# Kernel tuning notes

Measured on AMD Instinct MI355X. Metric: run time of the kernel, lower is better.

The kernel has to match this reference:

```python
import jax, jax.numpy as jnp
import numpy as np

N_NODES = 100000
FEAT_DIM = 256
EMBED_DIM = 256
BATCH = 50000
NUM_SAMPLE = 10


def setup_inputs() -> dict:
    key = jax.random.key(0)
    k1, k2, k3, k4 = jax.random.split(key, 4)
    features = jax.random.normal(k1, (N_NODES, FEAT_DIM), dtype=jnp.float32)
    # weight: [embed_dim, 2*feat_dim] (gcn=False path), xavier-like scale
    weight = jax.random.normal(k2, (EMBED_DIM, 2 * FEAT_DIM), dtype=jnp.float32)
    weight = weight * jnp.sqrt(2.0 / (EMBED_DIM + 2 * FEAT_DIM))
    nodes = jax.random.randint(k3, (BATCH,), 0, N_NODES, dtype=jnp.int64)
    neigh_idx = jax.random.randint(k4, (BATCH, NUM_SAMPLE), 0, N_NODES, dtype=jnp.int64)
    return {"features": features, "weight": weight, "nodes": nodes, "neigh_idx": neigh_idx}


def reference(features, weight, nodes, neigh_idx):
    # MeanAggregator: gather sampled neighbor feats and average over samples
    neigh_feats = features[neigh_idx].mean(axis=1)          # [B, F]
    self_feats = features[nodes]                             # [B, F]
    combined = jnp.concatenate([self_feats, neigh_feats], axis=1)  # [B, 2F]
    # weight.mm(combined.t()) -> [embed_dim, B], then relu
    out = jax.nn.relu(weight @ combined.T)
    return out
```

## Files before the change

### kernel.cpp

```cpp
#include <hip/hip_runtime.h>

#define FEAT   256
#define K2     512
#define NNODES 100000
#define BATCH  50000
#define NS     10
#define EMBED  256
#define BN     32
#define NBLK   ((BATCH + BN - 1) / BN)

typedef __attribute__((ext_vector_type(8))) __bf16         bf16x8;
typedef __attribute__((ext_vector_type(8))) unsigned short ushort8;
typedef __attribute__((ext_vector_type(4))) float          f32x4;
typedef __attribute__((ext_vector_type(2))) float          f32x2;
typedef __attribute__((ext_vector_type(2))) int            i32x2;
typedef __attribute__((ext_vector_type(4))) int            i32x4;

static __device__ __forceinline__ unsigned short f2bf(float x) {
    unsigned int u = __builtin_bit_cast(unsigned int, x);
    u += 0x7FFFu + ((u >> 16) & 1u);
    return (unsigned short)(u >> 16);
}

__global__ void fconv_kernel(const float* __restrict__ f,
                             unsigned char* __restrict__ f8) {
    int i = blockIdx.x * blockDim.x + threadIdx.x;
    const f32x4* src = (const f32x4*)(f + (size_t)i * 8);
    f32x4 a = src[0], b = src[1];
    int u0 = 0, u1 = 0;
    u0 = __builtin_amdgcn_cvt_pk_fp8_f32(a[0], a[1], u0, false);
    u0 = __builtin_amdgcn_cvt_pk_fp8_f32(a[2], a[3], u0, true);
    u1 = __builtin_amdgcn_cvt_pk_fp8_f32(b[0], b[1], u1, false);
    u1 = __builtin_amdgcn_cvt_pk_fp8_f32(b[2], b[3], u1, true);
    i32x2 p; p[0] = u0; p[1] = u1;
    ((i32x2*)f8)[i] = p;
}

__global__ void wpack_kernel(const float* __restrict__ w,
                             unsigned short* __restrict__ wp) {
    int c    = blockIdx.x * blockDim.x + threadIdx.x;
    int lane = c & 63;
    int ks   = (c >> 6) & 1;
    int mblk = (c >> 7) & 15;
    int kt   = c >> 11;
    int row  = mblk * 16 + (lane & 15);
    int col  = kt * 64 + ks * 32 + (lane >> 4) * 8;
    const f32x4* src = (const f32x4*)(w + row * K2 + col);
    f32x4 a = src[0], b = src[1];
    ushort8 h;
    h[0]=f2bf(a[0]); h[1]=f2bf(a[1]); h[2]=f2bf(a[2]); h[3]=f2bf(a[3]);
    h[4]=f2bf(b[0]); h[5]=f2bf(b[1]); h[6]=f2bf(b[2]); h[7]=f2bf(b[3]);
    ((ushort8*)wp)[c] = h;
}

__global__ __launch_bounds__(512, 4) void gemm_hyb(
    const float* __restrict__ features,
    const unsigned char* __restrict__ f8,
    const unsigned short* __restrict__ wp,
    const int* __restrict__ nodes,
    const int* __restrict__ neigh,
    float* __restrict__ out) {

    __shared__ __align__(16) unsigned short lB[BN * K2];

    const int tid = threadIdx.x;
    const int nb0 = blockIdx.x * BN;
    const int r   = tid >> 4;
    const int p   = tid & 15;
    const int rx  = r & 7;
    const int n   = min(nb0 + r, BATCH - 1);

    {
        const int node0 = nodes[n];
        const f32x4* s0 = (const f32x4*)(features + (size_t)node0 * FEAT + p * 16);
        f32x4 x0 = s0[0], x1 = s0[1], x2 = s0[2], x3 = s0[3];
        ushort8 a, b;
        a[0]=f2bf(x0[0]); a[1]=f2bf(x0[1]); a[2]=f2bf(x0[2]); a[3]=f2bf(x0[3]);
        a[4]=f2bf(x1[0]); a[5]=f2bf(x1[1]); a[6]=f2bf(x1[2]); a[7]=f2bf(x1[3]);
        b[0]=f2bf(x2[0]); b[1]=f2bf(x2[1]); b[2]=f2bf(x2[2]); b[3]=f2bf(x2[3]);
        b[4]=f2bf(x3[0]); b[5]=f2bf(x3[1]); b[6]=f2bf(x3[2]); b[7]=f2bf(x3[3]);
        const int g = p >> 2, i0 = (p & 3) * 2;
        unsigned short* dst = lB + r * K2 + g * 64;
        *(ushort8*)&dst[((i0    ) ^ rx) * 8] = a;
        *(ushort8*)&dst[((i0 + 1) ^ rx) * 8] = b;
    }

    {
        int idx[NS];
        #pragma unroll
        for (int s = 0; s < NS; ++s) idx[s] = neigh[n * NS + s];

        float acc[16];
        #pragma unroll
        for (int e = 0; e < 16; ++e) acc[e] = 0.f;

        #pragma unroll
        for (int s = 0; s < NS; ++s) {
            i32x4 v = *(const i32x4*)(f8 + (size_t)idx[s] * FEAT + p * 16);
            #pragma unroll
            for (int q = 0; q < 4; ++q) {
                f32x2 lo = __builtin_amdgcn_cvt_pk_f32_fp8(v[q], false);
                f32x2 hi = __builtin_amdgcn_cvt_pk_f32_fp8(v[q], true);
                acc[q * 4 + 0] += lo[0];
                acc[q * 4 + 1] += lo[1];
                acc[q * 4 + 2] += hi[0];
                acc[q * 4 + 3] += hi[1];
            }
        }
        ushort8 a, b;
        #pragma unroll
        for (int e = 0; e < 8; ++e) {
            a[e] = f2bf(acc[e]     * 0.1f);
            b[e] = f2bf(acc[8 + e] * 0.1f);
        }
        const int g = 4 + (p >> 2), i0 = (p & 3) * 2;
        unsigned short* dst = lB + r * K2 + g * 64;
        *(ushort8*)&dst[((i0    ) ^ rx) * 8] = a;
        *(ushort8*)&dst[((i0 + 1) ^ rx) * 8] = b;
    }
    __syncthreads();

    const int w    = tid >> 6;
    const int lane = tid & 63;
    const int lr   = lane & 15;
    const int lg   = lane >> 4;

    f32x4 facc[2][2] = {};

    #pragma unroll
    for (int kt = 0; kt < 8; ++kt) {
        bf16x8 af[2][2], bfr[2][2];
        #pragma unroll
        for (int i = 0; i < 2; ++i)
            #pragma unroll
            for (int ks = 0; ks < 2; ++ks)
                af[i][ks] = *(const bf16x8*)(wp +
                    ((((kt * 16 + w * 2 + i) * 2 + ks) * 64 + lane) << 3));
        #pragma unroll
        for (int j = 0; j < 2; ++j) {
            const int rb = j * 16 + lr;
            #pragma unroll
            for (int ks = 0; ks < 2; ++ks) {
                int cc = kt * 8 + ((ks * 4 + lg) ^ (rb & 7));
                bfr[j][ks] = *(const bf16x8*)&lB[rb * K2 + cc * 8];
            }
        }
        #pragma unroll
        for (int ks = 0; ks < 2; ++ks)
            #pragma unroll
            for (int i = 0; i < 2; ++i)
                #pragma unroll
                for (int j = 0; j < 2; ++j)
                    facc[i][j] = __builtin_amdgcn_mfma_f32_16x16x32_bf16(
                        af[i][ks], bfr[j][ks], facc[i][j], 0, 0, 0);
    }

    #pragma unroll
    for (int j = 0; j < 2; ++j) {
        const int n2 = nb0 + j * 16 + lr;
        if (n2 < BATCH) {
            #pragma unroll
            for (int i = 0; i < 2; ++i) {
                int m0 = w * 32 + i * 16 + lg * 4;
                #pragma unroll
                for (int rg = 0; rg < 4; ++rg) {
                    float v = facc[i][j][rg];
                    v = v > 0.f ? v : 0.f;
                    __builtin_nontemporal_store(v, &out[(size_t)(m0 + rg) * BATCH + n2]);
                }
            }
        }
    }
}

__global__ __launch_bounds__(512, 4) void gemm_f32(
    const float* __restrict__ features,
    const unsigned short* __restrict__ wp,
    const int* __restrict__ nodes,
    const int* __restrict__ neigh,
    float* __restrict__ out) {

    __shared__ __align__(16) unsigned short lB[BN * K2];

    const int tid = threadIdx.x;
    const int nb0 = blockIdx.x * BN;
    const int r  = tid >> 4;
    const int h  = tid & 15;
    const int rx = r & 7;
    const int n  = min(nb0 + r, BATCH - 1);

    int node0 = nodes[n];
    int nidx[NS];
    #pragma unroll
    for (int s = 0; s < NS; ++s) nidx[s] = neigh[n * NS + s];

    {
        const f32x4* s0 = (const f32x4*)(features + (size_t)node0 * FEAT + h * 16);
        f32x4 x0 = s0[0], x1 = s0[1], x2 = s0[2], x3 = s0[3];
        ushort8 a, b;
        a[0]=f2bf(x0[0]); a[1]=f2bf(x0[1]); a[2]=f2bf(x0[2]); a[3]=f2bf(x0[3]);
        a[4]=f2bf(x1[0]); a[5]=f2bf(x1[1]); a[6]=f2bf(x1[2]); a[7]=f2bf(x1[3]);
        b[0]=f2bf(x2[0]); b[1]=f2bf(x2[1]); b[2]=f2bf(x2[2]); b[3]=f2bf(x2[3]);
        b[4]=f2bf(x3[0]); b[5]=f2bf(x3[1]); b[6]=f2bf(x3[2]); b[7]=f2bf(x3[3]);
        const int g = h >> 2, i0 = (h & 3) * 2;
        unsigned short* dst = lB + r * K2 + g * 64;
        *(ushort8*)&dst[((i0    ) ^ rx) * 8] = a;
        *(ushort8*)&dst[((i0 + 1) ^ rx) * 8] = b;
    }
    {
        float acc[16];
        #pragma unroll
        for (int e = 0; e < 16; ++e) acc[e] = 0.f;
        #pragma unroll
        for (int s = 0; s < NS; ++s) {
            const f32x4* pp = (const f32x4*)(features + (size_t)nidx[s] * FEAT + h * 16);
            f32x4 x0 = pp[0], x1 = pp[1], x2 = pp[2], x3 = pp[3];
            #pragma unroll
            for (int e = 0; e < 4; ++e) {
                acc[e]      += x0[e];
                acc[4 + e]  += x1[e];
                acc[8 + e]  += x2[e];
                acc[12 + e] += x3[e];
            }
        }
        ushort8 aa, bb;
        #pragma unroll
        for (int e = 0; e < 8; ++e) {
            aa[e] = f2bf(acc[e]     * 0.1f);
            bb[e] = f2bf(acc[8 + e] * 0.1f);
        }
        const int g = 4 + (h >> 2), i0 = (h & 3) * 2;
        unsigned short* dst = lB + r * K2 + g * 64;
        *(ushort8*)&dst[((i0    ) ^ rx) * 8] = aa;
        *(ushort8*)&dst[((i0 + 1) ^ rx) * 8] = bb;
    }
    __syncthreads();

    const int w    = tid >> 6;
    const int lane = tid & 63;
    const int lr   = lane & 15;
    const int lg   = lane >> 4;

    f32x4 facc[2][2] = {};
    #pragma unroll
    for (int kt = 0; kt < 8; ++kt) {
        bf16x8 af[2][2], bfr[2][2];
        #pragma unroll
        for (int i = 0; i < 2; ++i)
            #pragma unroll
            for (int ks = 0; ks < 2; ++ks)
                af[i][ks] = *(const bf16x8*)(wp +
                    ((((kt * 16 + w * 2 + i) * 2 + ks) * 64 + lane) << 3));
        #pragma unroll
        for (int j = 0; j < 2; ++j) {
            const int rb = j * 16 + lr;
            #pragma unroll
            for (int ks = 0; ks < 2; ++ks) {
                int cc = kt * 8 + ((ks * 4 + lg) ^ (rb & 7));
                bfr[j][ks] = *(const bf16x8*)&lB[rb * K2 + cc * 8];
            }
        }
        #pragma unroll
        for (int ks = 0; ks < 2; ++ks)
            #pragma unroll
            for (int i = 0; i < 2; ++i)
                #pragma unroll
                for (int j = 0; j < 2; ++j)
                    facc[i][j] = __builtin_amdgcn_mfma_f32_16x16x32_bf16(
                        af[i][ks], bfr[j][ks], facc[i][j], 0, 0, 0);
    }
    #pragma unroll
    for (int j = 0; j < 2; ++j) {
        const int n2 = nb0 + j * 16 + lr;
        if (n2 < BATCH) {
            #pragma unroll
            for (int i = 0; i < 2; ++i) {
                int m0 = w * 32 + i * 16 + lg * 4;
                #pragma unroll
                for (int rg = 0; rg < 4; ++rg) {
                    float v = facc[i][j][rg];
                    v = v > 0.f ? v : 0.f;
                    __builtin_nontemporal_store(v, &out[(size_t)(m0 + rg) * BATCH + n2]);
                }
            }
        }
    }
}

extern "C" void kernel_launch(void* const* d_in, const int* in_sizes, int n_in,
                              void* d_out, int out_size, void* d_ws, size_t ws_size,
                              hipStream_t stream) {
    const float* features = (const float*)d_in[0];
    const float* weight   = (const float*)d_in[1];
    const int*   nodes    = (const int*)d_in[2];
    const int*   neigh    = (const int*)d_in[3];
    float* out = (float*)d_out;

    unsigned short* wp = (unsigned short*)d_ws;
    unsigned char*  f8 = (unsigned char*)(wp + (size_t)EMBED * K2);

    const size_t need = (size_t)EMBED * K2 * 2 + (size_t)NNODES * FEAT;

    wpack_kernel<<<(EMBED * K2 / 8) / 256, 256, 0, stream>>>(weight, wp);

    if (ws_size >= need) {
        fconv_kernel<<<(NNODES * FEAT / 8) / 256, 256, 0, stream>>>(features, f8);
        gemm_hyb<<<NBLK, 512, 0, stream>>>(features, f8, wp, nodes, neigh, out);
    } else {
        gemm_f32<<<NBLK, 512, 0, stream>>>(features, wp, nodes, neigh, out);
    }
}
```

Before: 74.20 us.

## Double batch tile to 64 columns with 1024-thread blocks in hybrid GEMM

The hybrid gather+GEMM kernel now handles 64 batch columns per block with 1024 threads (16 waves). Each wave owns one 16-row slice of the output embedding and all four 16-column batch tiles, rather than a 32x32 tile. This halves the number of blocks and the total number of times the packed weight is reloaded, and each wave's weight fragment is reused across four batch tiles. The costs are 64 KB of LDS per block and fewer, larger blocks, which reduces occupancy and makes the tail coarser. The fallback f32 kernel keeps its 32-column tiling.

```diff
diff --git a/kernel.cpp b/kernel.cpp
--- a/kernel.cpp
+++ b/kernel.cpp
@@ -6,7 +6,7 @@
 #define BATCH  50000
 #define NS     10
 #define EMBED  256
-#define BN     32
+#define BN     64
 #define NBLK   ((BATCH + BN - 1) / BN)
 
 typedef __attribute__((ext_vector_type(8))) __bf16         bf16x8;
@@ -53,7 +53,7 @@
     ((ushort8*)wp)[c] = h;
 }
 
-__global__ __launch_bounds__(512, 4) void gemm_hyb(
+__global__ __launch_bounds__(1024, 4) void gemm_hyb(
     const float* __restrict__ features,
     const unsigned char* __restrict__ f8,
     const unsigned short* __restrict__ wp,
@@ -125,49 +125,38 @@
     const int lr   = lane & 15;
     const int lg   = lane >> 4;
 
-    f32x4 facc[2][2] = {};
+    f32x4 facc[4] = {};
 
     #pragma unroll
     for (int kt = 0; kt < 8; ++kt) {
-        bf16x8 af[2][2], bfr[2][2];
-        #pragma unroll
-        for (int i = 0; i < 2; ++i)
-            #pragma unroll
-            for (int ks = 0; ks < 2; ++ks)
-                af[i][ks] = *(const bf16x8*)(wp +
-                    ((((kt * 16 + w * 2 + i) * 2 + ks) * 64 + lane) << 3));
-        #pragma unroll
-        for (int j = 0; j < 2; ++j) {
+        bf16x8 af[2];
+        #pragma unroll
+        for (int ks = 0; ks < 2; ++ks)
+            af[ks] = *(const bf16x8*)(wp +
+                ((((kt * 16 + w) * 2 + ks) * 64 + lane) << 3));
+        #pragma unroll
+        for (int j = 0; j < 4; ++j) {
             const int rb = j * 16 + lr;
             #pragma unroll
             for (int ks = 0; ks < 2; ++ks) {
                 int cc = kt * 8 + ((ks * 4 + lg) ^ (rb & 7));
-                bfr[j][ks] = *(const bf16x8*)&lB[rb * K2 + cc * 8];
-            }
-        }
-        #pragma unroll
-        for (int ks = 0; ks < 2; ++ks)
-            #pragma unroll
-            for (int i = 0; i < 2; ++i)
-                #pragma unroll
-                for (int j = 0; j < 2; ++j)
-                    facc[i][j] = __builtin_amdgcn_mfma_f32_16x16x32_bf16(
-                        af[i][ks], bfr[j][ks], facc[i][j], 0, 0, 0);
-    }
-
-    #pragma unroll
-    for (int j = 0; j < 2; ++j) {
+                bf16x8 bfr = *(const bf16x8*)&lB[rb * K2 + cc * 8];
+                facc[j] = __builtin_amdgcn_mfma_f32_16x16x32_bf16(
+                    af[ks], bfr, facc[j], 0, 0, 0);
+            }
+        }
+    }
+
+    const int m0 = w * 16 + lg * 4;
+    #pragma unroll
+    for (int j = 0; j < 4; ++j) {
         const int n2 = nb0 + j * 16 + lr;
         if (n2 < BATCH) {
             #pragma unroll
-            for (int i = 0; i < 2; ++i) {
-                int m0 = w * 32 + i * 16 + lg * 4;
-                #pragma unroll
-                for (int rg = 0; rg < 4; ++rg) {
-                    float v = facc[i][j][rg];
-                    v = v > 0.f ? v : 0.f;
-                    __builtin_nontemporal_store(v, &out[(size_t)(m0 + rg) * BATCH + n2]);
-                }
+            for (int rg = 0; rg < 4; ++rg) {
+                float v = facc[j][rg];
+                v = v > 0.f ? v : 0.f;
+                __builtin_nontemporal_store(v, &out[(size_t)(m0 + rg) * BATCH + n2]);
             }
         }
     }
@@ -180,10 +169,10 @@
     const int* __restrict__ neigh,
     float* __restrict__ out) {
 
-    __shared__ __align__(16) unsigned short lB[BN * K2];
+    __shared__ __align__(16) unsigned short lB[32 * K2];
 
     const int tid = threadIdx.x;
-    const int nb0 = blockIdx.x * BN;
+    const int nb0 = blockIdx.x * 32;
     const int r  = tid >> 4;
     const int h  = tid & 15;
     const int rx = r & 7;
@@ -305,8 +294,8 @@
 
     if (ws_size >= need) {
         fconv_kernel<<<(NNODES * FEAT / 8) / 256, 256, 0, stream>>>(features, f8);
-        gemm_hyb<<<NBLK, 512, 0, stream>>>(features, f8, wp, nodes, neigh, out);
+        gemm_hyb<<<NBLK, 1024, 0, stream>>>(features, f8, wp, nodes, neigh, out);
     } else {
-        gemm_f32<<<NBLK, 512, 0, stream>>>(features, wp, nodes, neigh, out);
-    }
-}
+        gemm_f32<<<(BATCH + 31) / 32, 512, 0, stream>>>(features, wp, nodes, neigh, out);
+    }
+}
```

After: 79.37 us. 1.07x slower.

## Merge prep kernels, prefetch first weight tile before barrier, raise occupancy hint

Applied to the files above, without the earlier changes.

Folds the fp8 feature conversion and the bf16 weight packing into one prep launch, removing one kernel launch and its gap. In the GEMM kernel, the first k-tile of packed weights is loaded into registers before the shared-memory barrier so that load overlaps the gather phase. The launch-bounds occupancy hint goes from 4 to 6 waves-per-SIMD target, which may force register limits and spills.

```diff
diff --git a/kernel.cpp b/kernel.cpp
--- a/kernel.cpp
+++ b/kernel.cpp
@@ -8,6 +8,8 @@
 #define EMBED  256
 #define BN     32
 #define NBLK   ((BATCH + BN - 1) / BN)
+#define FCONV_BLKS (NNODES * FEAT / 8 / 256)
+#define WPACK_BLKS 64
 
 typedef __attribute__((ext_vector_type(8))) __bf16         bf16x8;
 typedef __attribute__((ext_vector_type(8))) unsigned short ushort8;
@@ -22,23 +24,8 @@
     return (unsigned short)(u >> 16);
 }
 
-__global__ void fconv_kernel(const float* __restrict__ f,
-                             unsigned char* __restrict__ f8) {
-    int i = blockIdx.x * blockDim.x + threadIdx.x;
-    const f32x4* src = (const f32x4*)(f + (size_t)i * 8);
-    f32x4 a = src[0], b = src[1];
-    int u0 = 0, u1 = 0;
-    u0 = __builtin_amdgcn_cvt_pk_fp8_f32(a[0], a[1], u0, false);
-    u0 = __builtin_amdgcn_cvt_pk_fp8_f32(a[2], a[3], u0, true);
-    u1 = __builtin_amdgcn_cvt_pk_fp8_f32(b[0], b[1], u1, false);
-    u1 = __builtin_amdgcn_cvt_pk_fp8_f32(b[2], b[3], u1, true);
-    i32x2 p; p[0] = u0; p[1] = u1;
-    ((i32x2*)f8)[i] = p;
-}
-
-__global__ void wpack_kernel(const float* __restrict__ w,
-                             unsigned short* __restrict__ wp) {
-    int c    = blockIdx.x * blockDim.x + threadIdx.x;
+static __device__ __forceinline__ void wpack_body(int c, const float* __restrict__ w,
+                                                  unsigned short* __restrict__ wp) {
     int lane = c & 63;
     int ks   = (c >> 6) & 1;
     int mblk = (c >> 7) & 15;
@@ -53,7 +40,33 @@
     ((ushort8*)wp)[c] = h;
 }
 
-__global__ __launch_bounds__(512, 4) void gemm_hyb(
+__global__ void prep_kernel(const float* __restrict__ f,
+                            unsigned char* __restrict__ f8,
+                            const float* __restrict__ w,
+                            unsigned short* __restrict__ wp) {
+    const int bid = blockIdx.x;
+    if (bid < FCONV_BLKS) {
+        int i = bid * 256 + threadIdx.x;
+        const f32x4* src = (const f32x4*)(f + (size_t)i * 8);
+        f32x4 a = src[0], b = src[1];
+        int u0 = 0, u1 = 0;
+        u0 = __builtin_amdgcn_cvt_pk_fp8_f32(a[0], a[1], u0, false);
+        u0 = __builtin_amdgcn_cvt_pk_fp8_f32(a[2], a[3], u0, true);
+        u1 = __builtin_amdgcn_cvt_pk_fp8_f32(b[0], b[1], u1, false);
+        u1 = __builtin_amdgcn_cvt_pk_fp8_f32(b[2], b[3], u1, true);
+        i32x2 p; p[0] = u0; p[1] = u1;
+        ((i32x2*)f8)[i] = p;
+    } else {
+        wpack_body((bid - FCONV_BLKS) * 256 + threadIdx.x, w, wp);
+    }
+}
+
+__global__ void wpack_kernel(const float* __restrict__ w,
+                             unsigned short* __restrict__ wp) {
+    wpack_body(blockIdx.x * 256 + threadIdx.x, w, wp);
+}
+
+__global__ __launch_bounds__(512, 6) void gemm_hyb(
     const float* __restrict__ features,
     const unsigned char* __restrict__ f8,
     const unsigned short* __restrict__ wp,
@@ -118,12 +131,20 @@
         *(ushort8*)&dst[((i0    ) ^ rx) * 8] = a;
         *(ushort8*)&dst[((i0 + 1) ^ rx) * 8] = b;
     }
-    __syncthreads();
 
     const int w    = tid >> 6;
     const int lane = tid & 63;
-    const int lr   = lane & 15;
-    const int lg   = lane >> 4;
+    bf16x8 af0[2][2];
+    #pragma unroll
+    for (int i = 0; i < 2; ++i)
+        #pragma unroll
+        for (int ks = 0; ks < 2; ++ks)
+            af0[i][ks] = *(const bf16x8*)(wp +
+                ((((w * 2 + i) * 2 + ks) * 64 + lane) << 3));
+    __syncthreads();
+
+    const int lr = lane & 15;
+    const int lg = lane >> 4;
 
     f32x4 facc[2][2] = {};
 
@@ -134,8 +155,9 @@
         for (int i = 0; i < 2; ++i)
             #pragma unroll
             for (int ks = 0; ks < 2; ++ks)
-                af[i][ks] = *(const bf16x8*)(wp +
-                    ((((kt * 16 + w * 2 + i) * 2 + ks) * 64 + lane) << 3));
+                af[i][ks] = (kt == 0) ? af0[i][ks]
+                    : *(const bf16x8*)(wp +
+                        ((((kt * 16 + w * 2 + i) * 2 + ks) * 64 + lane) << 3));
         #pragma unroll
         for (int j = 0; j < 2; ++j) {
             const int rb = j * 16 + lr;
@@ -301,12 +323,11 @@
 
     const size_t need = (size_t)EMBED * K2 * 2 + (size_t)NNODES * FEAT;
 
-    wpack_kernel<<<(EMBED * K2 / 8) / 256, 256, 0, stream>>>(weight, wp);
-
     if (ws_size >= need) {
-        fconv_kernel<<<(NNODES * FEAT / 8) / 256, 256, 0, stream>>>(features, f8);
+        prep_kernel<<<FCONV_BLKS + WPACK_BLKS, 256, 0, stream>>>(features, f8, weight, wp);
         gemm_hyb<<<NBLK, 512, 0, stream>>>(features, f8, wp, nodes, neigh, out);
     } else {
+        wpack_kernel<<<WPACK_BLKS, 256, 0, stream>>>(weight, wp);
         gemm_f32<<<NBLK, 512, 0, stream>>>(features, wp, nodes, neigh, out);
     }
 }
```

Result: slower. 92.69 us (+24.9%).
